# Performance work log

Hardware: AMD Instinct MI355X
Metric: run time of the kernel (lower is better)

The kernel has to match this reference:

```python
import jax, jax.numpy as jnp
import numpy as np

B, S, D, H = 2, 2048, 1024, 16
EPS = 1e-7  # keras backend epsilon

def setup_inputs() -> dict:
    key = jax.random.key(0)
    ks = jax.random.split(key, 5)
    x = jax.random.normal(ks[0], (B, S, D), dtype=jnp.float32)
    # mem_mask convention: attend where mem_mask == 0 (causal here)
    i = jnp.arange(S)
    causal = (i[None, :] > i[:, None]).astype(jnp.float32)  # 1 = masked
    mem_mask = jnp.broadcast_to(causal[None, None], (B, 1, S, S))
    Wqkv = jax.random.normal(ks[1], (D, 3 * D), dtype=jnp.float32) * (D ** -0.5)
    W_out = jax.random.normal(ks[2], (D, D), dtype=jnp.float32) * (D ** -0.5)
    b_out = jnp.zeros((D,), dtype=jnp.float32)
    scale = jnp.ones((D,), dtype=jnp.float32)
    gate = jax.random.normal(ks[3], (D,), dtype=jnp.float32) * 0.02
    return {"x": x, "mem_mask": mem_mask, "Wqkv": Wqkv, "W_out": W_out,
            "b_out": b_out, "scale": scale, "gate": gate}

def reference(x, mem_mask, Wqkv, W_out, b_out, scale, gate):
    b, s, d = x.shape
    dh = d // H
    h = jnp.einsum('bsd,de->bse', x, Wqkv)
    q, k, v = jnp.split(h, 3, axis=-1)
    def split_heads(t):
        return t.reshape(b, s, H, dh).transpose(0, 2, 1, 3)  # [B,H,S,dh]
    q, k, v = split_heads(q), split_heads(k), split_heads(v)
    q = q * (dh ** -0.5)
    logits = jnp.einsum('bhqd,bhkd->bhqk', q, k)
    logits = logits * (mem_mask == 0.0).astype(logits.dtype)
    weights = jax.nn.relu(logits)
    o = jnp.einsum('bhqk,bhkd->bhqd', weights, v)
    o = o.transpose(0, 2, 1, 3).reshape(b, s, d)  # combine heads
    # Gated RMSNorm
    ms = jnp.mean(o * o, axis=-1, keepdims=True)
    o = scale * o * jax.lax.rsqrt(ms + EPS) * jax.nn.sigmoid(gate * o)
    return jnp.einsum('bsd,de->bse', o, W_out) + b_out
```

## Files before the change

kernel.cpp:

```cpp
#include <hip/hip_runtime.h>
#include <hip/hip_bf16.h>

typedef unsigned short u16;
typedef __attribute__((ext_vector_type(8))) short bf16x8;
typedef __attribute__((ext_vector_type(4))) short short4v;
typedef __attribute__((ext_vector_type(4))) float floatx4;
typedef __attribute__((ext_vector_type(2))) unsigned uint2v;
typedef __attribute__((ext_vector_type(4))) unsigned uint4v;

__device__ __forceinline__ float bf2f(u16 u) {
    unsigned v = ((unsigned)u) << 16;
    return __builtin_bit_cast(float, v);
}
__device__ __forceinline__ u16 f2bf(float f) {
    unsigned u = __builtin_bit_cast(unsigned, f);
    u += 0x7fffu + ((u >> 16) & 1u);
    return (u16)(u >> 16);
}

#define GLDS16(g, l)                                                             \
    __builtin_amdgcn_global_load_lds(                                            \
        (const __attribute__((address_space(1))) void*)(g),                      \
        (__attribute__((address_space(3))) void*)(l), 16, 0, 0)

__device__ __forceinline__ uint2v pl32(unsigned a, unsigned b) {
#if __has_builtin(__builtin_amdgcn_permlane32_swap)
    auto r = __builtin_amdgcn_permlane32_swap(a, b, false, false);
    uint2v o; o.x = (unsigned)r[0]; o.y = (unsigned)r[1]; return o;
#else
    unsigned as = (unsigned)__shfl_xor((int)a, 32, 64);
    unsigned bs = (unsigned)__shfl_xor((int)b, 32, 64);
    const bool hi = (threadIdx.x & 32) != 0;
    uint2v o; o.x = hi ? bs : a; o.y = hi ? b : as; return o;
#endif
}
__device__ __forceinline__ uint2v pl16(unsigned a, unsigned b) {
#if __has_builtin(__builtin_amdgcn_permlane16_swap)
    auto r = __builtin_amdgcn_permlane16_swap(a, b, false, false);
    uint2v o; o.x = (unsigned)r[0]; o.y = (unsigned)r[1]; return o;
#else
    unsigned as = (unsigned)__shfl_xor((int)a, 16, 64);
    unsigned bs = (unsigned)__shfl_xor((int)b, 16, 64);
    const bool odd = (threadIdx.x & 16) != 0;
    uint2v o; o.x = odd ? bs : a; o.y = odd ? b : as; return o;
#endif
}

__global__ __launch_bounds__(256) void prep(const float* __restrict__ x, u16* __restrict__ xb,
                                            const float* __restrict__ Wqkv, u16* __restrict__ WqkvT,
                                            const float* __restrict__ Wout, u16* __restrict__ WoutT) {
    __shared__ u16 t[32][33];
    int blk = blockIdx.x;
    if (blk < 4096) {
        const int i = blk * 256 + threadIdx.x;
        const floatx4 v = ((const floatx4*)x)[i];
        short4v o;
#pragma unroll
        for (int j = 0; j < 4; ++j) o[j] = (short)f2bf(v[j]);
        ((short4v*)xb)[i] = o;
        return;
    }
    const float* in; u16* out; int R, C, bx, by;
    if (blk < 4096 + 3072) { blk -= 4096; in = Wqkv; out = WqkvT; R = 1024; C = 3072; bx = blk % 96; by = blk / 96; }
    else                   { blk -= 7168; in = Wout; out = WoutT; R = 1024; C = 1024; bx = blk & 31; by = blk >> 5; }
    const int c0 = bx * 32, r0 = by * 32;
    const int xx = threadIdx.x & 31, yy = threadIdx.x >> 5;
#pragma unroll
    for (int i = 0; i < 32; i += 8) t[yy + i][xx] = f2bf(in[(size_t)(r0 + yy + i) * C + c0 + xx]);
    __syncthreads();
#pragma unroll
    for (int i = 0; i < 32; i += 8) out[(size_t)(c0 + yy + i) * R + r0 + xx] = t[xx][yy + i];
}

template <int TM, int BN, bool BIAS, typename OUT, bool VT>
__global__ __launch_bounds__(256) void gemm_bt(const u16* __restrict__ A, const u16* __restrict__ Bt,
                                               OUT* __restrict__ C, const float* __restrict__ bias,
                                               u16* __restrict__ vtp, int M, int N, int K) {
    constexpr int MI = TM / 32;
    constexpr int NJ = BN / 32;
    __shared__ u16 sA[TM * 32];
    __shared__ u16 sB[BN * 32];
    const int tid = threadIdx.x;
    const int lane = tid & 63, wave = tid >> 6;
    const int l15 = lane & 15, quad = lane >> 4;
    const int row0 = blockIdx.y * TM, col0 = blockIdx.x * BN;
    const int wm = (wave & 1) * (TM / 2), wn = (wave >> 1) * (BN / 2);
    const int c_ = (tid & 3) << 3;
    floatx4 acc[MI][NJ] = {};
    for (int k0 = 0; k0 < K; k0 += 32) {
#pragma unroll
        for (int it = 0; it < BN / 64; ++it) {
            const int idx = it * 256 + tid;
            const int r = idx >> 2;
            GLDS16(Bt + (size_t)(col0 + r) * K + k0 + c_, sB + idx * 8);
        }
#pragma unroll
        for (int it = 0; it < TM / 64; ++it) {
            const int idx = it * 256 + tid;
            const int r = idx >> 2;
            GLDS16(A + (size_t)(row0 + r) * K + k0 + c_, sA + idx * 8);
        }
        __syncthreads();
        bf16x8 af[MI], bfr[NJ];
#pragma unroll
        for (int i = 0; i < MI; ++i) af[i] = *(const bf16x8*)(sA + (wm + i * 16 + l15) * 32 + quad * 8);
#pragma unroll
        for (int j = 0; j < NJ; ++j) bfr[j] = *(const bf16x8*)(sB + (wn + j * 16 + l15) * 32 + quad * 8);
#pragma unroll
        for (int i = 0; i < MI; ++i)
#pragma unroll
            for (int j = 0; j < NJ; ++j)
                acc[i][j] = __builtin_amdgcn_mfma_f32_16x16x32_bf16(af[i], bfr[j], acc[i][j], 0, 0, 0);
        __syncthreads();
    }
#pragma unroll
    for (int i = 0; i < MI; ++i) {
#pragma unroll
        for (int j = 0; j < NJ; ++j) {
            const int col = col0 + wn + j * 16 + l15;
            const int row = row0 + wm + i * 16 + quad * 4;
            const float b = BIAS ? bias[col] : 0.f;
            short4v pk;
#pragma unroll
            for (int r = 0; r < 4; ++r) {
                const float v = acc[i][j][r] + b;
                if constexpr (sizeof(OUT) == 2)
                    C[(size_t)(row + r) * N + col] = (OUT)f2bf(v);
                else
                    C[(size_t)(row + r) * N + col] = (OUT)v;
                if constexpr (VT) pk[r] = (short)f2bf(v * 0.125f);
            }
            if constexpr (VT) {
                if (col0 >= 2048) {
                    const int bb = row >> 11, s = row & 2047;
                    const int hd = (col - 2048) >> 6, dh = col & 63;
                    *(short4v*)(vtp + ((size_t)(bb * 16 + hd) * 64 + dh) * 2048 + s) = pk;
                }
            }
        }
    }
}

__device__ __forceinline__ uint2v pack_relu(floatx4 s, bool diag, int kgb, int qg) {
    float v0 = fmaxf(s[0], 0.f), v1 = fmaxf(s[1], 0.f);
    float v2 = fmaxf(s[2], 0.f), v3 = fmaxf(s[3], 0.f);
    if (diag) {
        if (kgb + 0 > qg) v0 = 0.f;
        if (kgb + 1 > qg) v1 = 0.f;
        if (kgb + 2 > qg) v2 = 0.f;
        if (kgb + 3 > qg) v3 = 0.f;
    }
    uint2v p;
    p.x = ((__builtin_bit_cast(unsigned, v0) + 0x8000u) >> 16) |
          ((__builtin_bit_cast(unsigned, v1) + 0x8000u) & 0xffff0000u);
    p.y = ((__builtin_bit_cast(unsigned, v2) + 0x8000u) >> 16) |
          ((__builtin_bit_cast(unsigned, v3) + 0x8000u) & 0xffff0000u);
    return p;
}

__device__ __forceinline__ bf16x8 pfrag(uint2v A, uint2v B) {
    uint2v gx = pl32(A.x, B.x);
    uint2v dx = pl16(gx.x, gx.y);
    uint2v gy = pl32(A.y, B.y);
    uint2v dy = pl16(gy.x, gy.y);
    uint4v w; w.x = dx.x; w.y = dy.x; w.z = dx.y; w.w = dy.y;
    return __builtin_bit_cast(bf16x8, w);
}

__global__ __launch_bounds__(256) void relu_attn(const u16* __restrict__ h, const u16* __restrict__ vt,
                                                 float* __restrict__ o) {
    __shared__ u16 sK[3][64 * 64];
    __shared__ u16 sV[3][64 * 64];
    const int bid = blockIdx.x;
    const int pr = bid >> 5;
    const int bh = bid & 31;
    const int b = bh >> 4, hd = bh & 15;
    const int qtl = pr, qth = 31 - pr;
    const int tid = threadIdx.x, lane = tid & 63, wave = tid >> 6;
    const int l15 = lane & 15, quad = lane >> 4;
    const int swz = l15 & 7;

    bf16x8 qfl[2], qfh[2];
    {
        const u16* ql = h + (size_t)(b * 2048 + qtl * 64 + wave * 16 + l15) * 3072 + hd * 64;
        const u16* qh = h + (size_t)(b * 2048 + qth * 64 + wave * 16 + l15) * 3072 + hd * 64;
#pragma unroll
        for (int ks = 0; ks < 2; ++ks) {
            qfl[ks] = *(const bf16x8*)(ql + ks * 32 + quad * 8);
            qfh[ks] = *(const bf16x8*)(qh + ks * 32 + quad * 8);
        }
    }

    floatx4 accl[4] = {}, acch[4] = {};
    const u16* kbase = h + (size_t)(b * 2048) * 3072 + 1024 + hd * 64;
    const u16* vbase = vt + (size_t)bh * 64 * 2048;
    const int qg = wave * 16 + l15;

    const u16* kq[2]; const u16* vq[2]; int lo[2];
#pragma unroll
    for (int it = 0; it < 2; ++it) {
        const int idx = it * 256 + tid;
        const int r = idx >> 3;
        const int cg = (idx & 7) ^ (r & 7);
        kq[it] = kbase + (size_t)r * 3072 + cg * 8;
        vq[it] = vbase + (size_t)r * 2048 + cg * 8;
        lo[it] = idx * 8;
    }
    auto stage = [&](int bufi) {
#pragma unroll
        for (int it = 0; it < 2; ++it) {
            GLDS16(kq[it], &sK[bufi][lo[it]]);
            GLDS16(vq[it], &sV[bufi][lo[it]]);
            kq[it] += 64 * 3072;
            vq[it] += 64;
        }
    };

    stage(0);
    stage(1);
    int bc = 0, bn = 1, bs = 2;

    for (int kc = 0; kc <= qth; ++kc) {
        if (kc < qth) asm volatile("s_waitcnt vmcnt(4)" ::: "memory");
        else          asm volatile("s_waitcnt vmcnt(0)" ::: "memory");
        __builtin_amdgcn_s_barrier();
        asm volatile("" ::: "memory");
        __builtin_amdgcn_sched_barrier(0);
        if (kc + 2 <= qth) stage(bs);

        const u16* sKb = sK[bc];
        const u16* sVb = sV[bc];
        const bool lact = (kc <= qtl);
        const floatx4 z = {0.f, 0.f, 0.f, 0.f};
        __builtin_amdgcn_s_setprio(1);
        uint2v ph[4], pl_[4];
#pragma unroll
        for (int mt = 0; mt < 4; ++mt) {
            const int R = mt * 16 + l15;
            const int cq = quad ^ swz;
            const bf16x8 kf0 = *(const bf16x8*)(sKb + R * 64 + cq * 8);
            const bf16x8 kf1 = *(const bf16x8*)(sKb + R * 64 + (cq ^ 4) * 8);
            const int kgb = mt * 16 + quad * 4;
            floatx4 s = __builtin_amdgcn_mfma_f32_16x16x32_bf16(kf0, qfh[0], z, 0, 0, 0);
            s = __builtin_amdgcn_mfma_f32_16x16x32_bf16(kf1, qfh[1], s, 0, 0, 0);
            ph[mt] = pack_relu(s, kc == qth, kgb, qg);
            if (lact) {
                floatx4 t = __builtin_amdgcn_mfma_f32_16x16x32_bf16(kf0, qfl[0], z, 0, 0, 0);
                t = __builtin_amdgcn_mfma_f32_16x16x32_bf16(kf1, qfl[1], t, 0, 0, 0);
                pl_[mt] = pack_relu(t, kc == qtl, kgb, qg);
            }
        }
#pragma unroll
        for (int kb = 0; kb < 2; ++kb) {
            const bf16x8 pfh = pfrag(ph[2 * kb], ph[2 * kb + 1]);
            bf16x8 pfl;
            if (lact) pfl = pfrag(pl_[2 * kb], pl_[2 * kb + 1]);
#pragma unroll
            for (int nt = 0; nt < 4; ++nt) {
                const int cv = ((kb << 2) | quad) ^ swz;
                const bf16x8 vf = *(const bf16x8*)(sVb + (nt * 16 + l15) * 64 + cv * 8);
                acch[nt] = __builtin_amdgcn_mfma_f32_16x16x32_bf16(pfh, vf, acch[nt], 0, 0, 0);
                if (lact) accl[nt] = __builtin_amdgcn_mfma_f32_16x16x32_bf16(pfl, vf, accl[nt], 0, 0, 0);
            }
        }
        __builtin_amdgcn_s_setprio(0);
        int t_ = bc; bc = bn; bn = bs; bs = t_;
    }
#pragma unroll
    for (int nt = 0; nt < 4; ++nt) {
        const int col = hd * 64 + nt * 16 + l15;
        const int rl = qtl * 64 + wave * 16 + quad * 4;
        const int rh = qth * 64 + wave * 16 + quad * 4;
#pragma unroll
        for (int r = 0; r < 4; ++r) {
            o[(size_t)(b * 2048 + rl + r) * 1024 + col] = accl[nt][r];
            o[(size_t)(b * 2048 + rh + r) * 1024 + col] = acch[nt][r];
        }
    }
}

__global__ __launch_bounds__(256) void rms_gate(const float* __restrict__ o, const float* __restrict__ scale,
                                                const float* __restrict__ gate, u16* __restrict__ out) {
    const int row = blockIdx.x;
    const int tid = threadIdx.x;
    const floatx4* op = (const floatx4*)(o + (size_t)row * 1024);
    floatx4 v = op[tid];
    float ss = v[0] * v[0] + v[1] * v[1] + v[2] * v[2] + v[3] * v[3];
#pragma unroll
    for (int m = 32; m >= 1; m >>= 1) ss += __shfl_xor(ss, m, 64);
    __shared__ float red[4];
    if ((tid & 63) == 0) red[tid >> 6] = ss;
    __syncthreads();
    const float ms = (red[0] + red[1] + red[2] + red[3]) * (1.0f / 1024.0f);
    const float inv = rsqrtf(ms + 1e-7f);
    const int c = tid * 4;
#pragma unroll
    for (int j = 0; j < 4; ++j) {
        const float s = scale[c + j];
        const float g = gate[c + j];
        const float x = v[j];
        const float sig = 1.0f / (1.0f + __expf(-g * x));
        out[(size_t)row * 1024 + c + j] = f2bf(s * x * inv * sig);
    }
}

extern "C" void kernel_launch(void* const* d_in, const int* in_sizes, int n_in,
                              void* d_out, int out_size, void* d_ws, size_t ws_size,
                              hipStream_t stream) {
    const float* x     = (const float*)d_in[0];
    const float* Wqkv  = (const float*)d_in[2];
    const float* Wout  = (const float*)d_in[3];
    const float* bout  = (const float*)d_in[4];
    const float* scale = (const float*)d_in[5];
    const float* gate  = (const float*)d_in[6];
    float* out = (float*)d_out;

    char* p = (char*)d_ws;
    u16* xb    = (u16*)p; p += (size_t)4096 * 1024 * 2;
    u16* h     = (u16*)p; p += (size_t)4096 * 3072 * 2;
    u16* vt    = (u16*)p; p += (size_t)32 * 64 * 2048 * 2;
    u16* WqkvT = (u16*)p; p += (size_t)3072 * 1024 * 2;
    u16* WoutT = (u16*)p; p += (size_t)1024 * 1024 * 2;
    float* oat = (float*)p; p += (size_t)4096 * 1024 * 4;
    u16* onorm = (u16*)p; p += (size_t)4096 * 1024 * 2;

    prep<<<8192, 256, 0, stream>>>(x, xb, Wqkv, WqkvT, Wout, WoutT);
    gemm_bt<128, 128, false, u16, true><<<dim3(24, 32), 256, 0, stream>>>(xb, WqkvT, h, nullptr, vt, 4096, 3072, 1024);
    relu_attn<<<512, 256, 0, stream>>>(h, vt, oat);
    rms_gate<<<4096, 256, 0, stream>>>(oat, scale, gate, onorm);
    gemm_bt<128, 64, true, float, false><<<dim3(16, 32), 256, 0, stream>>>(onorm, WoutT, out, bout, nullptr, 4096, 1024, 1024);
}
```

Baseline: 216.2 us.

## Restructure relu attention to split keys across waves with LDS reduction

The attention kernel changes from paired low/high query tiles per block, with each wave owning 16 query rows, to one 64-row query tile per block. Each of the four waves takes a 32-key slice of a 128-key chunk, and the per-wave partial outputs are summed through LDS at the end. The grid doubles to 1024 blocks with launch bounds allowing two blocks per CU, and staging moves from triple to double buffering over larger K/V chunks. This aims to improve load balance and MFMA density, at the cost of a cross-wave reduction, a full vmcnt(0) wait each iteration, and lost prefetch depth.

```diff
diff --git a/kernel.cpp b/kernel.cpp
--- a/kernel.cpp
+++ b/kernel.cpp
@@ -167,114 +167,130 @@
     return __builtin_bit_cast(bf16x8, w);
 }
 
-__global__ __launch_bounds__(256) void relu_attn(const u16* __restrict__ h, const u16* __restrict__ vt,
-                                                 float* __restrict__ o) {
-    __shared__ u16 sK[3][64 * 64];
-    __shared__ u16 sV[3][64 * 64];
+__global__ __launch_bounds__(256, 2) void relu_attn(const u16* __restrict__ h, const u16* __restrict__ vt,
+                                                    float* __restrict__ o) {
+    union SM {
+        struct { u16 K[2][128 * 64]; u16 V[2][64 * 128]; } kv;
+        float red[4][64 * 68];
+    };
+    __shared__ SM sm;
     const int bid = blockIdx.x;
     const int pr = bid >> 5;
     const int bh = bid & 31;
+    const int qt64 = 31 - pr;
     const int b = bh >> 4, hd = bh & 15;
-    const int qtl = pr, qth = 31 - pr;
     const int tid = threadIdx.x, lane = tid & 63, wave = tid >> 6;
     const int l15 = lane & 15, quad = lane >> 4;
-    const int swz = l15 & 7;
-
-    bf16x8 qfl[2], qfh[2];
-    {
-        const u16* ql = h + (size_t)(b * 2048 + qtl * 64 + wave * 16 + l15) * 3072 + hd * 64;
-        const u16* qh = h + (size_t)(b * 2048 + qth * 64 + wave * 16 + l15) * 3072 + hd * 64;
-#pragma unroll
-        for (int ks = 0; ks < 2; ++ks) {
-            qfl[ks] = *(const bf16x8*)(ql + ks * 32 + quad * 8);
-            qfh[ks] = *(const bf16x8*)(qh + ks * 32 + quad * 8);
-        }
-    }
-
-    floatx4 accl[4] = {}, acch[4] = {};
+    const int nc = (qt64 >> 1) + 1;
+
+    const int qrow0 = b * 2048 + qt64 * 64;
+    bf16x8 qf[4][2];
+#pragma unroll
+    for (int qt = 0; qt < 4; ++qt)
+#pragma unroll
+        for (int ks = 0; ks < 2; ++ks)
+            qf[qt][ks] = *(const bf16x8*)(h + (size_t)(qrow0 + qt * 16 + l15) * 3072 + hd * 64 + ks * 32 + quad * 8);
+
+    floatx4 acc[4][4] = {};
+
     const u16* kbase = h + (size_t)(b * 2048) * 3072 + 1024 + hd * 64;
     const u16* vbase = vt + (size_t)bh * 64 * 2048;
-    const int qg = wave * 16 + l15;
-
-    const u16* kq[2]; const u16* vq[2]; int lo[2];
-#pragma unroll
-    for (int it = 0; it < 2; ++it) {
+
+    const u16* kq[4]; const u16* vq[4]; int klo[4], vlo[4];
+#pragma unroll
+    for (int it = 0; it < 4; ++it) {
         const int idx = it * 256 + tid;
-        const int r = idx >> 3;
-        const int cg = (idx & 7) ^ (r & 7);
-        kq[it] = kbase + (size_t)r * 3072 + cg * 8;
-        vq[it] = vbase + (size_t)r * 2048 + cg * 8;
-        lo[it] = idx * 8;
+        { const int r = idx >> 3, c = idx & 7, cg = c ^ (r & 7);
+          kq[it] = kbase + (size_t)r * 3072 + cg * 8; klo[it] = idx * 8; }
+        { const int r = idx >> 4, c = idx & 15, cg = c ^ (r & 15);
+          vq[it] = vbase + (size_t)r * 2048 + cg * 8; vlo[it] = idx * 8; }
     }
     auto stage = [&](int bufi) {
 #pragma unroll
-        for (int it = 0; it < 2; ++it) {
-            GLDS16(kq[it], &sK[bufi][lo[it]]);
-            GLDS16(vq[it], &sV[bufi][lo[it]]);
-            kq[it] += 64 * 3072;
-            vq[it] += 64;
-        }
+        for (int it = 0; it < 4; ++it) { GLDS16(kq[it], &sm.kv.K[bufi][klo[it]]); kq[it] += 128 * 3072; }
+#pragma unroll
+        for (int it = 0; it < 4; ++it) { GLDS16(vq[it], &sm.kv.V[bufi][vlo[it]]); vq[it] += 128; }
     };
 
     stage(0);
-    stage(1);
-    int bc = 0, bn = 1, bs = 2;
-
-    for (int kc = 0; kc <= qth; ++kc) {
-        if (kc < qth) asm volatile("s_waitcnt vmcnt(4)" ::: "memory");
-        else          asm volatile("s_waitcnt vmcnt(0)" ::: "memory");
+    int buf = 0;
+    for (int kc = 0; kc < nc; ++kc) {
+        asm volatile("s_waitcnt vmcnt(0)" ::: "memory");
         __builtin_amdgcn_s_barrier();
         asm volatile("" ::: "memory");
         __builtin_amdgcn_sched_barrier(0);
-        if (kc + 2 <= qth) stage(bs);
-
-        const u16* sKb = sK[bc];
-        const u16* sVb = sV[bc];
-        const bool lact = (kc <= qtl);
+        if (kc + 1 < nc) stage(buf ^ 1);
+
+        const u16* sK = sm.kv.K[buf];
+        const u16* sV = sm.kv.V[buf];
+        __builtin_amdgcn_s_setprio(1);
+        bf16x8 kf[2][2];
+#pragma unroll
+        for (int kt = 0; kt < 2; ++kt)
+#pragma unroll
+            for (int ks = 0; ks < 2; ++ks) {
+                const int row = wave * 32 + kt * 16 + l15;
+                const int blk = (quad + ks * 4) ^ (row & 7);
+                kf[kt][ks] = *(const bf16x8*)(sK + row * 64 + blk * 8);
+            }
         const floatx4 z = {0.f, 0.f, 0.f, 0.f};
-        __builtin_amdgcn_s_setprio(1);
-        uint2v ph[4], pl_[4];
-#pragma unroll
-        for (int mt = 0; mt < 4; ++mt) {
-            const int R = mt * 16 + l15;
-            const int cq = quad ^ swz;
-            const bf16x8 kf0 = *(const bf16x8*)(sKb + R * 64 + cq * 8);
-            const bf16x8 kf1 = *(const bf16x8*)(sKb + R * 64 + (cq ^ 4) * 8);
-            const int kgb = mt * 16 + quad * 4;
-            floatx4 s = __builtin_amdgcn_mfma_f32_16x16x32_bf16(kf0, qfh[0], z, 0, 0, 0);
-            s = __builtin_amdgcn_mfma_f32_16x16x32_bf16(kf1, qfh[1], s, 0, 0, 0);
-            ph[mt] = pack_relu(s, kc == qth, kgb, qg);
-            if (lact) {
-                floatx4 t = __builtin_amdgcn_mfma_f32_16x16x32_bf16(kf0, qfl[0], z, 0, 0, 0);
-                t = __builtin_amdgcn_mfma_f32_16x16x32_bf16(kf1, qfl[1], t, 0, 0, 0);
-                pl_[mt] = pack_relu(t, kc == qtl, kgb, qg);
+        floatx4 s[2][4];
+#pragma unroll
+        for (int kt = 0; kt < 2; ++kt)
+#pragma unroll
+            for (int qt = 0; qt < 4; ++qt) {
+                floatx4 t = __builtin_amdgcn_mfma_f32_16x16x32_bf16(kf[kt][0], qf[qt][0], z, 0, 0, 0);
+                s[kt][qt] = __builtin_amdgcn_mfma_f32_16x16x32_bf16(kf[kt][1], qf[qt][1], t, 0, 0, 0);
             }
-        }
-#pragma unroll
-        for (int kb = 0; kb < 2; ++kb) {
-            const bf16x8 pfh = pfrag(ph[2 * kb], ph[2 * kb + 1]);
-            bf16x8 pfl;
-            if (lact) pfl = pfrag(pl_[2 * kb], pl_[2 * kb + 1]);
-#pragma unroll
-            for (int nt = 0; nt < 4; ++nt) {
-                const int cv = ((kb << 2) | quad) ^ swz;
-                const bf16x8 vf = *(const bf16x8*)(sVb + (nt * 16 + l15) * 64 + cv * 8);
-                acch[nt] = __builtin_amdgcn_mfma_f32_16x16x32_bf16(pfh, vf, acch[nt], 0, 0, 0);
-                if (lact) accl[nt] = __builtin_amdgcn_mfma_f32_16x16x32_bf16(pfl, vf, accl[nt], 0, 0, 0);
-            }
+        const bool last = (kc == nc - 1);
+        uint2v p[2][4];
+#pragma unroll
+        for (int kt = 0; kt < 2; ++kt)
+#pragma unroll
+            for (int qt = 0; qt < 4; ++qt)
+                p[kt][qt] = pack_relu(s[kt][qt], last,
+                                      kc * 128 + wave * 32 + kt * 16 + quad * 4,
+                                      qt64 * 64 + qt * 16 + l15);
+        bf16x8 vf[4];
+#pragma unroll
+        for (int nt = 0; nt < 4; ++nt) {
+            const int row = nt * 16 + l15;
+            const int blk = (wave * 4 + quad) ^ (row & 15);
+            vf[nt] = *(const bf16x8*)(sV + row * 128 + blk * 8);
+        }
+#pragma unroll
+        for (int qt = 0; qt < 4; ++qt) {
+            const bf16x8 pa = pfrag(p[0][qt], p[1][qt]);
+#pragma unroll
+            for (int nt = 0; nt < 4; ++nt)
+                acc[qt][nt] = __builtin_amdgcn_mfma_f32_16x16x32_bf16(pa, vf[nt], acc[qt][nt], 0, 0, 0);
         }
         __builtin_amdgcn_s_setprio(0);
-        int t_ = bc; bc = bn; bn = bs; bs = t_;
-    }
-#pragma unroll
-    for (int nt = 0; nt < 4; ++nt) {
-        const int col = hd * 64 + nt * 16 + l15;
-        const int rl = qtl * 64 + wave * 16 + quad * 4;
-        const int rh = qth * 64 + wave * 16 + quad * 4;
-#pragma unroll
-        for (int r = 0; r < 4; ++r) {
-            o[(size_t)(b * 2048 + rl + r) * 1024 + col] = accl[nt][r];
-            o[(size_t)(b * 2048 + rh + r) * 1024 + col] = acch[nt][r];
+        buf ^= 1;
+    }
+
+    __syncthreads();
+    float* rw = sm.red[wave];
+#pragma unroll
+    for (int qt = 0; qt < 4; ++qt)
+#pragma unroll
+        for (int nt = 0; nt < 4; ++nt) {
+            const int d = nt * 16 + l15, q = qt * 16 + quad * 4;
+            *(floatx4*)(rw + d * 68 + q) = acc[qt][nt];
+        }
+    __syncthreads();
+    {
+        const int d = lane;
+#pragma unroll
+        for (int j = 0; j < 4; ++j) {
+            const int q = wave * 16 + j * 4;
+            floatx4 a = *(const floatx4*)(sm.red[0] + d * 68 + q);
+            a += *(const floatx4*)(sm.red[1] + d * 68 + q);
+            a += *(const floatx4*)(sm.red[2] + d * 68 + q);
+            a += *(const floatx4*)(sm.red[3] + d * 68 + q);
+#pragma unroll
+            for (int jj = 0; jj < 4; ++jj)
+                o[(size_t)(qrow0 + q + jj) * 1024 + hd * 64 + d] = a[jj];
         }
     }
 }
@@ -326,7 +342,7 @@
 
     prep<<<8192, 256, 0, stream>>>(x, xb, Wqkv, WqkvT, Wout, WoutT);
     gemm_bt<128, 128, false, u16, true><<<dim3(24, 32), 256, 0, stream>>>(xb, WqkvT, h, nullptr, vt, 4096, 3072, 1024);
-    relu_attn<<<512, 256, 0, stream>>>(h, vt, oat);
+    relu_attn<<<1024, 256, 0, stream>>>(h, vt, oat);
     rms_gate<<<4096, 256, 0, stream>>>(oat, scale, gate, onorm);
     gemm_bt<128, 64, true, float, false><<<dim3(16, 32), 256, 0, stream>>>(onorm, WoutT, out, bout, nullptr, 4096, 1024, 1024);
 }
```

After: 203.1 us. 1.06x faster.
